# Kernel tuning notes

Hardware: AMD Instinct MI355X
Metric: run time of the kernel (lower is better)

## Reference

```python
import jax, jax.numpy as jnp
import numpy as np

EMB = 512
H1, H2 = 300, 100


def setup_inputs() -> dict:
    key = jax.random.key(0)
    ks = jax.random.split(key, 12)
    B, N, M = 2, 256, 256
    inp = {
        "action_embedding": jax.random.normal(ks[0], (B, EMB, N), jnp.float32),
        "anchor_embedding": jax.random.normal(ks[1], (B, EMB, M), jnp.float32),
        "action_points": jax.random.normal(ks[2], (B, 3, N), jnp.float32),
        "anchor_points": jax.random.normal(ks[3], (B, 3, M), jnp.float32),
        # MLPKernel params: Linear(1024,300), Linear(300,100), Linear(100,1), stored as [in,out]
        "W1": jax.random.normal(ks[4], (2 * EMB, H1), jnp.float32) / np.sqrt(2 * EMB),
        "b1": jax.random.normal(ks[5], (H1,), jnp.float32) * 0.01,
        "W2": jax.random.normal(ks[6], (H1, H2), jnp.float32) / np.sqrt(H1),
        "b2": jax.random.normal(ks[7], (H2,), jnp.float32) * 0.01,
        "W3": jax.random.normal(ks[8], (H2, 1), jnp.float32) / np.sqrt(H2),
        "b3": jax.random.normal(ks[9], (1,), jnp.float32) * 0.01,
    }
    return inp


def _pairwise_radii(Phi_A, Phi_B, W1, b1, W2, b2, W3, b3):
    # MLPKernel: softplus((mlp(cat(a,b)) + mlp(cat(b,a))) / 2) over all (n, m) pairs.
    # Split first linear: cat(x1,x2) @ W1 == x1 @ Wa + x2 @ Wb  (no [B,N,M,1024] materialization).
    F = Phi_A.shape[-1]
    Wa, Wb = W1[:F], W1[F:]
    hA_a = jnp.einsum('bnf,fh->bnh', Phi_A, Wa)
    hA_b = jnp.einsum('bnf,fh->bnh', Phi_A, Wb)
    hB_a = jnp.einsum('bmf,fh->bmh', Phi_B, Wa)
    hB_b = jnp.einsum('bmf,fh->bmh', Phi_B, Wb)

    def mlp_rest(h):  # h: [B,N,M,H1] pre-bias first-layer activations
        h = jax.nn.relu(h + b1)
        h = jax.nn.relu(jnp.einsum('bnmh,hk->bnmk', h, W2) + b2)
        return jnp.einsum('bnmk,ko->bnmo', h, W3) + b3

    v1 = mlp_rest(hA_a[:, :, None, :] + hB_b[:, None, :, :])  # mlp(cat(A_n, B_m))
    v2 = mlp_rest(hB_a[:, None, :, :] + hA_b[:, :, None, :])  # mlp(cat(B_m, A_n))
    return jax.nn.softplus((v1 + v2) * 0.5)[..., 0]  # [B,N,M]


def _multilaterate(P, R, W):
    # Vectorized estimate_p over batch b and query point n.
    # P: [B,M,3] anchor points, R: [B,N,M] estimated radii, W: [B,M] weights.
    M = P.shape[1]
    norm2 = jnp.sum(P * P, axis=-1)                      # [B,M]  (Pt @ P)
    d = norm2[:, None, :] - R ** 2                       # [B,N,M]  PtP - r^2
    a = jnp.einsum('bm,bnm,bmd->bnd', W, d, P) / M       # [B,N,3]
    WPPt = jnp.einsum('bm,bmd,bme->bde', W, P, P) / M    # [B,3,3]  mean(W * P Pt)
    mWd = jnp.einsum('bm,bnm->bn', W, d) / M             # [B,N]    mean(W * (PtP - r^2))
    c = jnp.einsum('bm,bmd->bd', W, P) / M               # [B,3]
    # B @ c with B = -2*mean(W*PPt) - mean(W*d)*I
    Bc = -2.0 * jnp.einsum('bde,be->bd', WPPt, c)[:, None, :] - mWd[..., None] * c[:, None, :]
    cc = jnp.sum(c * c, axis=-1)                         # [B]
    f = a + Bc + 2.0 * cc[:, None, None] * c[:, None, :]  # [B,N,3]
    PPt_mean = jnp.einsum('bmd,bme->bde', P, P) / M       # unweighted mean(PPt)
    H = -2.0 * PPt_mean + 2.0 * jnp.einsum('bd,be->bde', c, c)  # [B,3,3]
    Hinv = jnp.linalg.inv(H)
    q = -jnp.einsum('bde,bne->bnd', Hinv, f)
    return q + c[:, None, :]                              # [B,N,3]


def reference(action_embedding, anchor_embedding, action_points, anchor_points,
              W1, b1, W2, b2, W3, b3):
    P_A = jnp.transpose(action_points, (0, 2, 1))    # [B,N,3]
    P_B = jnp.transpose(anchor_points, (0, 2, 1))    # [B,M,3]
    Phi_A = jnp.transpose(action_embedding, (0, 2, 1))  # [B,N,F]
    Phi_B = jnp.transpose(anchor_embedding, (0, 2, 1))  # [B,M,F]
    B_weights = jnp.ones(Phi_B.shape[:2], dtype=Phi_B.dtype)
    R_est = _pairwise_radii(Phi_A, Phi_B, W1, b1, W2, b2, W3, b3)
    P_A_B_pred = _multilaterate(P_B, R_est, B_weights)  # [B,N,3]
    flow = jnp.transpose(P_A_B_pred - P_A, (0, 2, 1))   # [B,3,N] == full_flow (pred_weight=False)
    return flow
```

## Files before the change

### kernel.cpp

```cpp
#include <hip/hip_runtime.h>
#include <hip/hip_bf16.h>
#include <math.h>

#define EMB 512
#define H1 300
#define H2 100
#define NB 2
#define NN 256
#define MM 256

#define OFF_HAA 0
#define OFF_HAB 153600
#define OFF_HBA 307200
#define OFF_HBB 460800
#define OFF_S   614400
#define OFF_CST 616448
#define OFF_W2C 616512
#define OFF_B2P 634432
#define OFF_W3P 634544
#define OFF_ET  634656
#define OFF_W1T 896800
#define OFF_V   1060640

typedef __attribute__((ext_vector_type(8))) short bf16x8;
typedef __attribute__((ext_vector_type(4))) float f32x4;

static __device__ inline unsigned f2bfbits(float f) {
    union { float f; unsigned u; } v; v.f = f;
    return (v.u + 0x7fffu + ((v.u >> 16) & 1u)) >> 16;
}
static __device__ inline unsigned pack_bf2(float a, float b) {
    union { __hip_bfloat162 h; unsigned u; } cv;
    cv.h = __float22bfloat162_rn(make_float2(a, b));
    return cv.u;
}

__global__ void k_prep(const float* __restrict__ W2, const float* __restrict__ b2,
                       const float* __restrict__ W3, float* __restrict__ ws)
{
    unsigned short* W2c = (unsigned short*)(ws + OFF_W2C);
    int start = blockIdx.x * 256 + threadIdx.x;
    for (int idx = start; idx < 10*112*32; idx += gridDim.x * 256) {
        int c  = idx / 3584;
        int r  = idx - c * 3584;
        int j  = r >> 5;
        int kk = r & 31;
        int k  = c * 32 + kk;
        float v = (j < H2 && k < H1) ? W2[k * H2 + j] : 0.0f;
        W2c[idx] = (unsigned short)f2bfbits(v);
    }
    if (blockIdx.x == 0 && threadIdx.x < 112) {
        int j = threadIdx.x;
        ws[OFF_B2P + j] = (j < H2) ? b2[j] : 0.0f;
        ws[OFF_W3P + j] = (j < H2) ? W3[j] : 0.0f;
    }
}

__global__ void k_prepw1(const float* __restrict__ W1, float* __restrict__ ws)
{
    __shared__ float Tf[32 * 36];
    unsigned short* W1t = (unsigned short*)(ws + OFF_W1T);
    int h0 = blockIdx.x * 32, f0 = blockIdx.y * 32;
    int tid = threadIdx.x;
    int fr = tid >> 3, hc4 = (tid & 7) * 4;
    int hg = h0 + hc4;
    float4 v = make_float4(0.f, 0.f, 0.f, 0.f);
    if (hg < 600) {
        int half = (hg >= 300) ? 1 : 0;
        int hh = hg - half * 300;
        v = *(const float4*)&W1[(size_t)(half * EMB + f0 + fr) * H1 + hh];
    }
    *(float4*)&Tf[fr * 36 + hc4] = v;
    __syncthreads();
    int hr = tid >> 3, f4 = (tid & 7) * 4;
    float v0 = Tf[(f4 + 0) * 36 + hr];
    float v1 = Tf[(f4 + 1) * 36 + hr];
    float v2 = Tf[(f4 + 2) * 36 + hr];
    float v3 = Tf[(f4 + 3) * 36 + hr];
    uint2 pk = make_uint2(pack_bf2(v0, v1), pack_bf2(v2, v3));
    *(uint2*)&W1t[(size_t)(h0 + hr) * EMB + f0 + f4] = pk;
}

__global__ void k_prepe(const float* __restrict__ actE, const float* __restrict__ ancE,
                        float* __restrict__ ws)
{
    __shared__ float Tf[32 * 36];
    unsigned short* Et = (unsigned short*)(ws + OFF_ET);
    int f0 = blockIdx.x * 32, n0 = blockIdx.y * 32;
    int bs = blockIdx.z, b = bs >> 1, src = bs & 1;
    const float* E = (src == 0 ? actE : ancE) + (size_t)b * EMB * NN;
    int tid = threadIdx.x;
    int r = tid >> 3, c4 = (tid & 7) * 4;
    float4 v = *(const float4*)&E[(size_t)(f0 + r) * NN + n0 + c4];
    *(float4*)&Tf[r * 36 + c4] = v;
    __syncthreads();
    int nr = tid >> 3, f4 = (tid & 7) * 4;
    float v0 = Tf[(f4 + 0) * 36 + nr];
    float v1 = Tf[(f4 + 1) * 36 + nr];
    float v2 = Tf[(f4 + 2) * 36 + nr];
    float v3 = Tf[(f4 + 3) * 36 + nr];
    uint2 pk = make_uint2(pack_bf2(v0, v1), pack_bf2(v2, v3));
    *(uint2*)&Et[((size_t)(bs * NN) + n0 + nr) * EMB + f0 + f4] = pk;
}

__global__ void k_const(const float* __restrict__ anchor_pts, float* __restrict__ cst)
{
    int b = blockIdx.x;
    int m = threadIdx.x;
    float px = anchor_pts[b*3*MM + 0*MM + m];
    float py = anchor_pts[b*3*MM + 1*MM + m];
    float pz = anchor_pts[b*3*MM + 2*MM + m];
    float n2 = px*px + py*py + pz*pz;

    float v[13];
    v[0]=px; v[1]=py; v[2]=pz;
    v[3]=px*px; v[4]=px*py; v[5]=px*pz; v[6]=py*py; v[7]=py*pz; v[8]=pz*pz;
    v[9]=n2*px; v[10]=n2*py; v[11]=n2*pz; v[12]=n2;

    #pragma unroll
    for (int off = 32; off >= 1; off >>= 1) {
        #pragma unroll
        for (int i = 0; i < 13; i++) v[i] += __shfl_xor(v[i], off, 64);
    }
    __shared__ float red[4][13];
    int wave = threadIdx.x >> 6, lane = threadIdx.x & 63;
    if (lane == 0) {
        #pragma unroll
        for (int i = 0; i < 13; i++) red[wave][i] = v[i];
    }
    __syncthreads();
    if (threadIdx.x == 0) {
        float s[13];
        #pragma unroll
        for (int i = 0; i < 13; i++)
            s[i] = red[0][i] + red[1][i] + red[2][i] + red[3][i];
        const float invM = 1.0f / MM;
        float c0 = s[0]*invM, c1 = s[1]*invM, c2 = s[2]*invM;
        float Pxx = s[3]*invM, Pxy = s[4]*invM, Pxz = s[5]*invM;
        float Pyy = s[6]*invM, Pyz = s[7]*invM, Pzz = s[8]*invM;

        float H00 = -2.0f*Pxx + 2.0f*c0*c0;
        float H01 = -2.0f*Pxy + 2.0f*c0*c1;
        float H02 = -2.0f*Pxz + 2.0f*c0*c2;
        float H11 = -2.0f*Pyy + 2.0f*c1*c1;
        float H12 = -2.0f*Pyz + 2.0f*c1*c2;
        float H22 = -2.0f*Pzz + 2.0f*c2*c2;
        float H10 = H01, H20 = H02, H21 = H12;

        float det = H00*(H11*H22 - H12*H21)
                  - H01*(H10*H22 - H12*H20)
                  + H02*(H10*H21 - H11*H20);
        float id = 1.0f / det;
        float i00 = (H11*H22 - H12*H21)*id;
        float i01 = (H02*H21 - H01*H22)*id;
        float i02 = (H01*H12 - H02*H11)*id;
        float i10 = (H12*H20 - H10*H22)*id;
        float i11 = (H00*H22 - H02*H20)*id;
        float i12 = (H02*H10 - H00*H12)*id;
        float i20 = (H10*H21 - H11*H20)*id;
        float i21 = (H01*H20 - H00*H21)*id;
        float i22 = (H00*H11 - H01*H10)*id;

        float t0x = -2.0f*(Pxx*c0 + Pxy*c1 + Pxz*c2);
        float t0y = -2.0f*(Pxy*c0 + Pyy*c1 + Pyz*c2);
        float t0z = -2.0f*(Pxz*c0 + Pyz*c1 + Pzz*c2);
        float cc = c0*c0 + c1*c1 + c2*c2;

        float* C = cst + b*32;
        C[0]=c0; C[1]=c1; C[2]=c2;
        C[3]=i00; C[4]=i01; C[5]=i02;
        C[6]=i10; C[7]=i11; C[8]=i12;
        C[9]=i20; C[10]=i21; C[11]=i22;
        C[12]=t0x; C[13]=t0y; C[14]=t0z;
        C[15]=cc;
        C[16]=s[9]*invM; C[17]=s[10]*invM; C[18]=s[11]*invM; C[19]=s[12]*invM;
    }
}

__global__ __launch_bounds__(256) void k_hidden(
    float* __restrict__ ws, const float* __restrict__ b1)
{
    int bs = blockIdx.z, b = bs >> 1, src = bs & 1;
    int n0 = blockIdx.x * 32;
    int h0 = blockIdx.y * 64;
    const unsigned short* Et  = (const unsigned short*)(ws + OFF_ET)
                                + (size_t)(bs * NN) * EMB;
    const unsigned short* W1t = (const unsigned short*)(ws + OFF_W1T);
    float* outA = ws + (src == 0 ? OFF_HAA : OFF_HBA) + (size_t)b * NN * H1;
    float* outB = ws + (src == 0 ? OFF_HAB : OFF_HBB) + (size_t)b * NN * H1;

    __shared__ unsigned short EtL[32 * 40];
    __shared__ unsigned short W1tL[64 * 40];

    int tid = threadIdx.x;
    int lane = tid & 63, w = tid >> 6;
    int colj = lane & 15, quad = lane >> 4;
    int pt = w & 1, jt0 = (w >> 1) * 2;

    int erow = tid >> 3, es4 = (tid & 7) * 4;
    int wrow = tid >> 2, ws8 = (tid & 3) * 8;

    f32x4 acc[2];
    acc[0] = (f32x4){0.f,0.f,0.f,0.f};
    acc[1] = (f32x4){0.f,0.f,0.f,0.f};

    for (int c = 0; c < 16; c++) {
        int k0 = c * 32;
        uint2 ev = *(const uint2*)&Et[(size_t)(n0 + erow) * EMB + k0 + es4];
        uint4 wv = *(const uint4*)&W1t[(size_t)(h0 + wrow) * EMB + k0 + ws8];
        __syncthreads();
        *(uint2*)&EtL[erow * 40 + es4] = ev;
        *(uint4*)&W1tL[wrow * 40 + ws8] = wv;
        __syncthreads();

        bf16x8 af  = *(const bf16x8*)&EtL[(pt * 16 + colj) * 40 + quad * 8];
        bf16x8 bf0 = *(const bf16x8*)&W1tL[(jt0 * 16 + colj) * 40 + quad * 8];
        bf16x8 bf1 = *(const bf16x8*)&W1tL[((jt0 + 1) * 16 + colj) * 40 + quad * 8];
        acc[0] = __builtin_amdgcn_mfma_f32_16x16x32_bf16(af, bf0, acc[0], 0, 0, 0);
        acc[1] = __builtin_amdgcn_mfma_f32_16x16x32_bf16(af, bf1, acc[1], 0, 0, 0);
    }

    #pragma unroll
    for (int j2 = 0; j2 < 2; j2++) {
        int hg = h0 + (jt0 + j2) * 16 + colj;
        if (hg >= 600) continue;
        int hh = (hg < 300) ? hg : hg - 300;
        float* o = (hg < 300) ? outA : outB;
        float bias = (src == 0) ? b1[hh] : 0.0f;
        #pragma unroll
        for (int r = 0; r < 4; r++) {
            int n = n0 + pt * 16 + quad * 4 + r;
            o[(size_t)n * H1 + hh] = acc[j2][r] + bias;
        }
    }
}

__global__ __launch_bounds__(256) void k_pair(
    const float* __restrict__ ws_f, const float* __restrict__ b3p,
    float* __restrict__ V)
{
    int bz = blockIdx.z, b = bz >> 1, p = bz & 1;
    int n0 = blockIdx.y * 16, m0 = blockIdx.x * 16;
    int tid = threadIdx.x;
    int lane = tid & 63, w = tid >> 6;
    int colj = lane & 15, quad = lane >> 4;

    __shared__ float hAfL[16 * 36];
    __shared__ float hBfL[16 * 36];
    __shared__ short W2L[112 * 40];

    const unsigned short* W2c = (const unsigned short*)(ws_f + OFF_W2C);
    float b2v[7], w3v[7];
    #pragma unroll
    for (int jt = 0; jt < 7; jt++) {
        b2v[jt] = ws_f[OFF_B2P + jt * 16 + colj];
        w3v[jt] = ws_f[OFF_W3P + jt * 16 + colj];
    }
    float b3val = b3p[0];

    const float* srcX = ws_f + (p == 0 ? OFF_HAA : OFF_HAB) + (size_t)(b*NN + n0) * H1;
    const float* srcY = ws_f + (p == 0 ? OFF_HBB : OFF_HBA) + (size_t)(b*NN + m0) * H1;

    int sarr = tid >> 7;
    int srow = (tid >> 3) & 15;
    int sseg = tid & 7;
    const float* ssrc = (sarr ? srcY : srcX) + srow * H1;
    float* sdst = (sarr ? hBfL : hAfL) + srow * 36 + sseg * 4;

    f32x4 acc[4][7];
    #pragma unroll
    for (int i = 0; i < 4; i++)
        #pragma unroll
        for (int jt = 0; jt < 7; jt++)
            acc[i][jt] = (f32x4){0.f,0.f,0.f,0.f};

    for (int c = 0; c < 10; c++) {
        float4 sv = *(const float4*)&ssrc[c * 32 + sseg * 4];
        const uint4* wsrc4 = (const uint4*)W2c + c * 448;
        uint4 w0 = wsrc4[tid];
        uint4 w1 = wsrc4[(tid + 256) % 448];

        __syncthreads();
        *(float4*)sdst = sv;
        {
            int j = tid >> 2, q = tid & 3;
            *(uint4*)&W2L[j * 40 + q * 8] = w0;
            if (tid < 192) {
                int u2 = tid + 256;
                *(uint4*)&W2L[(u2 >> 2) * 40 + (u2 & 3) * 8] = w1;
            }
        }
        __syncthreads();

        float4 hb0 = *(const float4*)&hBfL[colj * 36 + quad * 8];
        float4 hb1 = *(const float4*)&hBfL[colj * 36 + quad * 8 + 4];
        bf16x8 bfr[7];
        #pragma unroll
        for (int jt = 0; jt < 7; jt++)
            bfr[jt] = *(const bf16x8*)&W2L[(jt * 16 + colj) * 40 + quad * 8];

        #pragma unroll
        for (int i = 0; i < 4; i++) {
            const float* xa = &hAfL[(w * 4 + i) * 36 + quad * 8];
            float4 ha0 = *(const float4*)&xa[0];
            float4 ha1 = *(const float4*)&xa[4];
            union { unsigned u[4]; bf16x8 v; } af;
            af.u[0] = pack_bf2(fmaxf(ha0.x + hb0.x, 0.f), fmaxf(ha0.y + hb0.y, 0.f));
            af.u[1] = pack_bf2(fmaxf(ha0.z + hb0.z, 0.f), fmaxf(ha0.w + hb0.w, 0.f));
            af.u[2] = pack_bf2(fmaxf(ha1.x + hb1.x, 0.f), fmaxf(ha1.y + hb1.y, 0.f));
            af.u[3] = pack_bf2(fmaxf(ha1.z + hb1.z, 0.f), fmaxf(ha1.w + hb1.w, 0.f));
            #pragma unroll
            for (int jt = 0; jt < 7; jt++)
                acc[i][jt] = __builtin_amdgcn_mfma_f32_16x16x32_bf16(
                    af.v, bfr[jt], acc[i][jt], 0, 0, 0);
        }
    }

    float vsum[4][4];
    #pragma unroll
    for (int i = 0; i < 4; i++)
        #pragma unroll
        for (int r = 0; r < 4; r++) vsum[i][r] = 0.0f;
    #pragma unroll
    for (int i = 0; i < 4; i++)
        #pragma unroll
        for (int jt = 0; jt < 7; jt++)
            #pragma unroll
            for (int r = 0; r < 4; r++)
                vsum[i][r] = fmaf(fmaxf(acc[i][jt][r] + b2v[jt], 0.f),
                                  w3v[jt], vsum[i][r]);

    #pragma unroll
    for (int i = 0; i < 4; i++)
        #pragma unroll
        for (int r = 0; r < 4; r++) {
            float v = vsum[i][r];
            v += __shfl_xor(v, 1, 16);
            v += __shfl_xor(v, 2, 16);
            v += __shfl_xor(v, 4, 16);
            v += __shfl_xor(v, 8, 16);
            vsum[i][r] = v;
        }

    if (colj == 0) {
        #pragma unroll
        for (int i = 0; i < 4; i++) {
            int n = n0 + w * 4 + i;
            float4 o;
            o.x = 0.5f * (vsum[i][0] + b3val);
            o.y = 0.5f * (vsum[i][1] + b3val);
            o.z = 0.5f * (vsum[i][2] + b3val);
            o.w = 0.5f * (vsum[i][3] + b3val);
            *(float4*)&V[(((size_t)p * NB + b) * NN + n) * MM + m0 + quad * 4] = o;
        }
    }
}

__global__ void k_red(const float* __restrict__ V, const float* __restrict__ ancP,
                      float* __restrict__ S)
{
    int b = blockIdx.y;
    int n = blockIdx.x * 16 + (threadIdx.x >> 4);
    int ml = threadIdx.x & 15;
    const float* v0 = V + (((size_t)0 * NB + b) * NN + n) * MM;
    const float* v1 = V + (((size_t)1 * NB + b) * NN + n) * MM;
    float s0 = 0.f, s1 = 0.f, s2 = 0.f, s3 = 0.f;
    #pragma unroll
    for (int k = 0; k < 16; k++) {
        int m = ml + k * 16;
        float x = v0[m] + v1[m];
        float R = fmaxf(x, 0.f) + log1pf(expf(-fabsf(x)));
        float r2 = R * R;
        float px = ancP[b*3*MM + 0*MM + m];
        float py = ancP[b*3*MM + 1*MM + m];
        float pz = ancP[b*3*MM + 2*MM + m];
        s0 = fmaf(r2, px, s0);
        s1 = fmaf(r2, py, s1);
        s2 = fmaf(r2, pz, s2);
        s3 += r2;
    }
    #pragma unroll
    for (int off = 8; off >= 1; off >>= 1) {
        s0 += __shfl_xor(s0, off, 16);
        s1 += __shfl_xor(s1, off, 16);
        s2 += __shfl_xor(s2, off, 16);
        s3 += __shfl_xor(s3, off, 16);
    }
    if (ml == 0) {
        float4 o = make_float4(s0, s1, s2, s3);
        *(float4*)&S[(size_t)(b * NN + n) * 4] = o;
    }
}

__global__ void k_final(const float* __restrict__ S, const float* __restrict__ cst,
                        const float* __restrict__ action_pts, float* __restrict__ out)
{
    int b = blockIdx.x;
    int n = threadIdx.x;
    const float* C = cst + b*32;
    float c0=C[0], c1=C[1], c2=C[2];
    float t0x=C[12], t0y=C[13], t0z=C[14];
    float cc=C[15];
    float SnP0=C[16], SnP1=C[17], SnP2=C[18], Sn=C[19];

    const float* sp = S + (b*NN + n) * 4;
    const float invM = 1.0f / MM;
    float a0 = SnP0 - sp[0]*invM;
    float a1 = SnP1 - sp[1]*invM;
    float a2 = SnP2 - sp[2]*invM;
    float mWd = Sn - sp[3]*invM;

    float f0 = a0 + t0x - mWd*c0 + 2.0f*cc*c0;
    float f1 = a1 + t0y - mWd*c1 + 2.0f*cc*c1;
    float f2 = a2 + t0z - mWd*c2 + 2.0f*cc*c2;

    float q0 = -(C[3]*f0 + C[4]*f1 + C[5]*f2);
    float q1 = -(C[6]*f0 + C[7]*f1 + C[8]*f2);
    float q2 = -(C[9]*f0 + C[10]*f1 + C[11]*f2);

    float p0 = q0 + c0, p1 = q1 + c1, p2 = q2 + c2;

    out[b*3*NN + 0*NN + n] = p0 - action_pts[b*3*NN + 0*NN + n];
    out[b*3*NN + 1*NN + n] = p1 - action_pts[b*3*NN + 1*NN + n];
    out[b*3*NN + 2*NN + n] = p2 - action_pts[b*3*NN + 2*NN + n];
}

extern "C" void kernel_launch(void* const* d_in, const int* in_sizes, int n_in,
                              void* d_out, int out_size, void* d_ws, size_t ws_size,
                              hipStream_t stream)
{
    const float* actE = (const float*)d_in[0];
    const float* ancE = (const float*)d_in[1];
    const float* actP = (const float*)d_in[2];
    const float* ancP = (const float*)d_in[3];
    const float* W1   = (const float*)d_in[4];
    const float* b1   = (const float*)d_in[5];
    const float* W2   = (const float*)d_in[6];
    const float* b2   = (const float*)d_in[7];
    const float* W3   = (const float*)d_in[8];
    const float* b3   = (const float*)d_in[9];
    float* ws  = (float*)d_ws;
    float* out = (float*)d_out;

    k_prep  <<<16, 256, 0, stream>>>(W2, b2, W3, ws);
    k_prepw1<<<dim3(20, 16), 256, 0, stream>>>(W1, ws);
    k_prepe <<<dim3(16, 8, 4), 256, 0, stream>>>(actE, ancE, ws);
    k_const <<<NB, 256, 0, stream>>>(ancP, ws + OFF_CST);
    k_hidden<<<dim3(8, 10, 4), 256, 0, stream>>>(ws, b1);
    k_pair  <<<dim3(16, 16, NB*2), 256, 0, stream>>>(ws, b3, ws + OFF_V);
    k_red   <<<dim3(16, NB), 256, 0, stream>>>(ws + OFF_V, ancP, ws + OFF_S);
    k_final <<<NB, 256, 0, stream>>>(ws + OFF_S, ws + OFF_CST, actP, out);
}
```

Baseline: 132.5 us.

## Merge prep kernels into one launch, fuse reduce+final, shrink hidden tile

Combines the four preprocessing kernels (W1 transpose, embedding transpose, W2 packing, anchor constants) into a single kernel dispatched by block index. It also folds the final multilateration solve into the radius reduction kernel, which removes a launch and the intermediate S buffer. The hidden-layer GEMM tile is halved along n, doubling the block count, with each wave doing one MFMA per step. The main aim is fewer kernel launches and better occupancy, at the cost of less reuse per block in k_hidden.

```diff
diff --git a/kernel.cpp b/kernel.cpp
--- a/kernel.cpp
+++ b/kernel.cpp
@@ -35,145 +35,144 @@
     return cv.u;
 }
 
-__global__ void k_prep(const float* __restrict__ W2, const float* __restrict__ b2,
-                       const float* __restrict__ W3, float* __restrict__ ws)
-{
-    unsigned short* W2c = (unsigned short*)(ws + OFF_W2C);
-    int start = blockIdx.x * 256 + threadIdx.x;
-    for (int idx = start; idx < 10*112*32; idx += gridDim.x * 256) {
-        int c  = idx / 3584;
-        int r  = idx - c * 3584;
-        int j  = r >> 5;
-        int kk = r & 31;
-        int k  = c * 32 + kk;
-        float v = (j < H2 && k < H1) ? W2[k * H2 + j] : 0.0f;
-        W2c[idx] = (unsigned short)f2bfbits(v);
-    }
-    if (blockIdx.x == 0 && threadIdx.x < 112) {
-        int j = threadIdx.x;
-        ws[OFF_B2P + j] = (j < H2) ? b2[j] : 0.0f;
-        ws[OFF_W3P + j] = (j < H2) ? W3[j] : 0.0f;
-    }
-}
-
-__global__ void k_prepw1(const float* __restrict__ W1, float* __restrict__ ws)
+__global__ __launch_bounds__(256) void k_setup(
+    const float* __restrict__ W1, const float* __restrict__ W2,
+    const float* __restrict__ b2, const float* __restrict__ W3,
+    const float* __restrict__ actE, const float* __restrict__ ancE,
+    const float* __restrict__ ancP, float* __restrict__ ws)
 {
     __shared__ float Tf[32 * 36];
-    unsigned short* W1t = (unsigned short*)(ws + OFF_W1T);
-    int h0 = blockIdx.x * 32, f0 = blockIdx.y * 32;
+    __shared__ float red[4][13];
+    int blk = blockIdx.x;
     int tid = threadIdx.x;
-    int fr = tid >> 3, hc4 = (tid & 7) * 4;
-    int hg = h0 + hc4;
-    float4 v = make_float4(0.f, 0.f, 0.f, 0.f);
-    if (hg < 600) {
-        int half = (hg >= 300) ? 1 : 0;
-        int hh = hg - half * 300;
-        v = *(const float4*)&W1[(size_t)(half * EMB + f0 + fr) * H1 + hh];
-    }
-    *(float4*)&Tf[fr * 36 + hc4] = v;
-    __syncthreads();
-    int hr = tid >> 3, f4 = (tid & 7) * 4;
-    float v0 = Tf[(f4 + 0) * 36 + hr];
-    float v1 = Tf[(f4 + 1) * 36 + hr];
-    float v2 = Tf[(f4 + 2) * 36 + hr];
-    float v3 = Tf[(f4 + 3) * 36 + hr];
-    uint2 pk = make_uint2(pack_bf2(v0, v1), pack_bf2(v2, v3));
-    *(uint2*)&W1t[(size_t)(h0 + hr) * EMB + f0 + f4] = pk;
-}
-
-__global__ void k_prepe(const float* __restrict__ actE, const float* __restrict__ ancE,
-                        float* __restrict__ ws)
-{
-    __shared__ float Tf[32 * 36];
-    unsigned short* Et = (unsigned short*)(ws + OFF_ET);
-    int f0 = blockIdx.x * 32, n0 = blockIdx.y * 32;
-    int bs = blockIdx.z, b = bs >> 1, src = bs & 1;
-    const float* E = (src == 0 ? actE : ancE) + (size_t)b * EMB * NN;
-    int tid = threadIdx.x;
-    int r = tid >> 3, c4 = (tid & 7) * 4;
-    float4 v = *(const float4*)&E[(size_t)(f0 + r) * NN + n0 + c4];
-    *(float4*)&Tf[r * 36 + c4] = v;
-    __syncthreads();
-    int nr = tid >> 3, f4 = (tid & 7) * 4;
-    float v0 = Tf[(f4 + 0) * 36 + nr];
-    float v1 = Tf[(f4 + 1) * 36 + nr];
-    float v2 = Tf[(f4 + 2) * 36 + nr];
-    float v3 = Tf[(f4 + 3) * 36 + nr];
-    uint2 pk = make_uint2(pack_bf2(v0, v1), pack_bf2(v2, v3));
-    *(uint2*)&Et[((size_t)(bs * NN) + n0 + nr) * EMB + f0 + f4] = pk;
-}
-
-__global__ void k_const(const float* __restrict__ anchor_pts, float* __restrict__ cst)
-{
-    int b = blockIdx.x;
-    int m = threadIdx.x;
-    float px = anchor_pts[b*3*MM + 0*MM + m];
-    float py = anchor_pts[b*3*MM + 1*MM + m];
-    float pz = anchor_pts[b*3*MM + 2*MM + m];
-    float n2 = px*px + py*py + pz*pz;
-
-    float v[13];
-    v[0]=px; v[1]=py; v[2]=pz;
-    v[3]=px*px; v[4]=px*py; v[5]=px*pz; v[6]=py*py; v[7]=py*pz; v[8]=pz*pz;
-    v[9]=n2*px; v[10]=n2*py; v[11]=n2*pz; v[12]=n2;
-
-    #pragma unroll
-    for (int off = 32; off >= 1; off >>= 1) {
-        #pragma unroll
-        for (int i = 0; i < 13; i++) v[i] += __shfl_xor(v[i], off, 64);
-    }
-    __shared__ float red[4][13];
-    int wave = threadIdx.x >> 6, lane = threadIdx.x & 63;
-    if (lane == 0) {
-        #pragma unroll
-        for (int i = 0; i < 13; i++) red[wave][i] = v[i];
-    }
-    __syncthreads();
-    if (threadIdx.x == 0) {
-        float s[13];
-        #pragma unroll
-        for (int i = 0; i < 13; i++)
-            s[i] = red[0][i] + red[1][i] + red[2][i] + red[3][i];
-        const float invM = 1.0f / MM;
-        float c0 = s[0]*invM, c1 = s[1]*invM, c2 = s[2]*invM;
-        float Pxx = s[3]*invM, Pxy = s[4]*invM, Pxz = s[5]*invM;
-        float Pyy = s[6]*invM, Pyz = s[7]*invM, Pzz = s[8]*invM;
-
-        float H00 = -2.0f*Pxx + 2.0f*c0*c0;
-        float H01 = -2.0f*Pxy + 2.0f*c0*c1;
-        float H02 = -2.0f*Pxz + 2.0f*c0*c2;
-        float H11 = -2.0f*Pyy + 2.0f*c1*c1;
-        float H12 = -2.0f*Pyz + 2.0f*c1*c2;
-        float H22 = -2.0f*Pzz + 2.0f*c2*c2;
-        float H10 = H01, H20 = H02, H21 = H12;
-
-        float det = H00*(H11*H22 - H12*H21)
-                  - H01*(H10*H22 - H12*H20)
-                  + H02*(H10*H21 - H11*H20);
-        float id = 1.0f / det;
-        float i00 = (H11*H22 - H12*H21)*id;
-        float i01 = (H02*H21 - H01*H22)*id;
-        float i02 = (H01*H12 - H02*H11)*id;
-        float i10 = (H12*H20 - H10*H22)*id;
-        float i11 = (H00*H22 - H02*H20)*id;
-        float i12 = (H02*H10 - H00*H12)*id;
-        float i20 = (H10*H21 - H11*H20)*id;
-        float i21 = (H01*H20 - H00*H21)*id;
-        float i22 = (H00*H11 - H01*H10)*id;
-
-        float t0x = -2.0f*(Pxx*c0 + Pxy*c1 + Pxz*c2);
-        float t0y = -2.0f*(Pxy*c0 + Pyy*c1 + Pyz*c2);
-        float t0z = -2.0f*(Pxz*c0 + Pyz*c1 + Pzz*c2);
-        float cc = c0*c0 + c1*c1 + c2*c2;
-
-        float* C = cst + b*32;
-        C[0]=c0; C[1]=c1; C[2]=c2;
-        C[3]=i00; C[4]=i01; C[5]=i02;
-        C[6]=i10; C[7]=i11; C[8]=i12;
-        C[9]=i20; C[10]=i21; C[11]=i22;
-        C[12]=t0x; C[13]=t0y; C[14]=t0z;
-        C[15]=cc;
-        C[16]=s[9]*invM; C[17]=s[10]*invM; C[18]=s[11]*invM; C[19]=s[12]*invM;
+
+    if (blk < 320) {
+        unsigned short* W1t = (unsigned short*)(ws + OFF_W1T);
+        int h0 = (blk % 20) * 32, f0 = (blk / 20) * 32;
+        int fr = tid >> 3, hc4 = (tid & 7) * 4;
+        int hg = h0 + hc4;
+        float4 v = make_float4(0.f, 0.f, 0.f, 0.f);
+        if (hg < 600) {
+            int half = (hg >= 300) ? 1 : 0;
+            int hh = hg - half * 300;
+            v = *(const float4*)&W1[(size_t)(half * EMB + f0 + fr) * H1 + hh];
+        }
+        *(float4*)&Tf[fr * 36 + hc4] = v;
+        __syncthreads();
+        int hr = tid >> 3, f4 = (tid & 7) * 4;
+        float v0 = Tf[(f4 + 0) * 36 + hr];
+        float v1 = Tf[(f4 + 1) * 36 + hr];
+        float v2 = Tf[(f4 + 2) * 36 + hr];
+        float v3 = Tf[(f4 + 3) * 36 + hr];
+        uint2 pk = make_uint2(pack_bf2(v0, v1), pack_bf2(v2, v3));
+        *(uint2*)&W1t[(size_t)(h0 + hr) * EMB + f0 + f4] = pk;
+    } else if (blk < 832) {
+        int i = blk - 320;
+        unsigned short* Et = (unsigned short*)(ws + OFF_ET);
+        int f0 = (i & 15) * 32;
+        int n0 = ((i >> 4) & 7) * 32;
+        int bs = i >> 7, b = bs >> 1, src = bs & 1;
+        const float* E = (src == 0 ? actE : ancE) + (size_t)b * EMB * NN;
+        int r = tid >> 3, c4 = (tid & 7) * 4;
+        float4 v = *(const float4*)&E[(size_t)(f0 + r) * NN + n0 + c4];
+        *(float4*)&Tf[r * 36 + c4] = v;
+        __syncthreads();
+        int nr = tid >> 3, f4 = (tid & 7) * 4;
+        float v0 = Tf[(f4 + 0) * 36 + nr];
+        float v1 = Tf[(f4 + 1) * 36 + nr];
+        float v2 = Tf[(f4 + 2) * 36 + nr];
+        float v3 = Tf[(f4 + 3) * 36 + nr];
+        uint2 pk = make_uint2(pack_bf2(v0, v1), pack_bf2(v2, v3));
+        *(uint2*)&Et[((size_t)(bs * NN) + n0 + nr) * EMB + f0 + f4] = pk;
+    } else if (blk < 848) {
+        int i = blk - 832;
+        unsigned short* W2c = (unsigned short*)(ws + OFF_W2C);
+        int start = i * 256 + tid;
+        for (int idx = start; idx < 10*112*32; idx += 16 * 256) {
+            int c  = idx / 3584;
+            int r  = idx - c * 3584;
+            int j  = r >> 5;
+            int kk = r & 31;
+            int k  = c * 32 + kk;
+            float v = (j < H2 && k < H1) ? W2[k * H2 + j] : 0.0f;
+            W2c[idx] = (unsigned short)f2bfbits(v);
+        }
+        if (i == 0 && tid < 112) {
+            int j = tid;
+            ws[OFF_B2P + j] = (j < H2) ? b2[j] : 0.0f;
+            ws[OFF_W3P + j] = (j < H2) ? W3[j] : 0.0f;
+        }
+    } else {
+        int b = blk - 848;
+        float* cst = ws + OFF_CST;
+        int m = tid;
+        float px = ancP[b*3*MM + 0*MM + m];
+        float py = ancP[b*3*MM + 1*MM + m];
+        float pz = ancP[b*3*MM + 2*MM + m];
+        float n2 = px*px + py*py + pz*pz;
+
+        float v[13];
+        v[0]=px; v[1]=py; v[2]=pz;
+        v[3]=px*px; v[4]=px*py; v[5]=px*pz; v[6]=py*py; v[7]=py*pz; v[8]=pz*pz;
+        v[9]=n2*px; v[10]=n2*py; v[11]=n2*pz; v[12]=n2;
+
+        #pragma unroll
+        for (int off = 32; off >= 1; off >>= 1) {
+            #pragma unroll
+            for (int q = 0; q < 13; q++) v[q] += __shfl_xor(v[q], off, 64);
+        }
+        int wave = tid >> 6, lane = tid & 63;
+        if (lane == 0) {
+            #pragma unroll
+            for (int q = 0; q < 13; q++) red[wave][q] = v[q];
+        }
+        __syncthreads();
+        if (tid == 0) {
+            float s[13];
+            #pragma unroll
+            for (int q = 0; q < 13; q++)
+                s[q] = red[0][q] + red[1][q] + red[2][q] + red[3][q];
+            const float invM = 1.0f / MM;
+            float c0 = s[0]*invM, c1 = s[1]*invM, c2 = s[2]*invM;
+            float Pxx = s[3]*invM, Pxy = s[4]*invM, Pxz = s[5]*invM;
+            float Pyy = s[6]*invM, Pyz = s[7]*invM, Pzz = s[8]*invM;
+
+            float H00 = -2.0f*Pxx + 2.0f*c0*c0;
+            float H01 = -2.0f*Pxy + 2.0f*c0*c1;
+            float H02 = -2.0f*Pxz + 2.0f*c0*c2;
+            float H11 = -2.0f*Pyy + 2.0f*c1*c1;
+            float H12 = -2.0f*Pyz + 2.0f*c1*c2;
+            float H22 = -2.0f*Pzz + 2.0f*c2*c2;
+            float H10 = H01, H20 = H02, H21 = H12;
+
+            float det = H00*(H11*H22 - H12*H21)
+                      - H01*(H10*H22 - H12*H20)
+                      + H02*(H10*H21 - H11*H20);
+            float id = 1.0f / det;
+            float i00 = (H11*H22 - H12*H21)*id;
+            float i01 = (H02*H21 - H01*H22)*id;
+            float i02 = (H01*H12 - H02*H11)*id;
+            float i10 = (H12*H20 - H10*H22)*id;
+            float i11 = (H00*H22 - H02*H20)*id;
+            float i12 = (H02*H10 - H00*H12)*id;
+            float i20 = (H10*H21 - H11*H20)*id;
+            float i21 = (H01*H20 - H00*H21)*id;
+            float i22 = (H00*H11 - H01*H10)*id;
+
+            float t0x = -2.0f*(Pxx*c0 + Pxy*c1 + Pxz*c2);
+            float t0y = -2.0f*(Pxy*c0 + Pyy*c1 + Pyz*c2);
+            float t0z = -2.0f*(Pxz*c0 + Pyz*c1 + Pzz*c2);
+            float cc = c0*c0 + c1*c1 + c2*c2;
+
+            float* C = cst + b*32;
+            C[0]=c0; C[1]=c1; C[2]=c2;
+            C[3]=i00; C[4]=i01; C[5]=i02;
+            C[6]=i10; C[7]=i11; C[8]=i12;
+            C[9]=i20; C[10]=i21; C[11]=i22;
+            C[12]=t0x; C[13]=t0y; C[14]=t0z;
+            C[15]=cc;
+            C[16]=s[9]*invM; C[17]=s[10]*invM; C[18]=s[11]*invM; C[19]=s[12]*invM;
+        }
     }
 }
 
@@ -181,7 +180,7 @@
     float* __restrict__ ws, const float* __restrict__ b1)
 {
     int bs = blockIdx.z, b = bs >> 1, src = bs & 1;
-    int n0 = blockIdx.x * 32;
+    int n0 = blockIdx.x * 16;
     int h0 = blockIdx.y * 64;
     const unsigned short* Et  = (const unsigned short*)(ws + OFF_ET)
                                 + (size_t)(bs * NN) * EMB;
@@ -189,48 +188,40 @@
     float* outA = ws + (src == 0 ? OFF_HAA : OFF_HBA) + (size_t)b * NN * H1;
     float* outB = ws + (src == 0 ? OFF_HAB : OFF_HBB) + (size_t)b * NN * H1;
 
-    __shared__ unsigned short EtL[32 * 40];
+    __shared__ unsigned short EtL[16 * 40];
     __shared__ unsigned short W1tL[64 * 40];
 
     int tid = threadIdx.x;
     int lane = tid & 63, w = tid >> 6;
     int colj = lane & 15, quad = lane >> 4;
-    int pt = w & 1, jt0 = (w >> 1) * 2;
-
-    int erow = tid >> 3, es4 = (tid & 7) * 4;
-    int wrow = tid >> 2, ws8 = (tid & 3) * 8;
-
-    f32x4 acc[2];
-    acc[0] = (f32x4){0.f,0.f,0.f,0.f};
-    acc[1] = (f32x4){0.f,0.f,0.f,0.f};
+
+    int er  = tid >> 4, ek2 = (tid & 15) * 2;
+    int wr  = tid >> 2, wk8 = (tid & 3) * 8;
+
+    f32x4 acc = (f32x4){0.f, 0.f, 0.f, 0.f};
 
     for (int c = 0; c < 16; c++) {
         int k0 = c * 32;
-        uint2 ev = *(const uint2*)&Et[(size_t)(n0 + erow) * EMB + k0 + es4];
-        uint4 wv = *(const uint4*)&W1t[(size_t)(h0 + wrow) * EMB + k0 + ws8];
-        __syncthreads();
-        *(uint2*)&EtL[erow * 40 + es4] = ev;
-        *(uint4*)&W1tL[wrow * 40 + ws8] = wv;
-        __syncthreads();
-
-        bf16x8 af  = *(const bf16x8*)&EtL[(pt * 16 + colj) * 40 + quad * 8];
-        bf16x8 bf0 = *(const bf16x8*)&W1tL[(jt0 * 16 + colj) * 40 + quad * 8];
-        bf16x8 bf1 = *(const bf16x8*)&W1tL[((jt0 + 1) * 16 + colj) * 40 + quad * 8];
-        acc[0] = __builtin_amdgcn_mfma_f32_16x16x32_bf16(af, bf0, acc[0], 0, 0, 0);
-        acc[1] = __builtin_amdgcn_mfma_f32_16x16x32_bf16(af, bf1, acc[1], 0, 0, 0);
-    }
-
-    #pragma unroll
-    for (int j2 = 0; j2 < 2; j2++) {
-        int hg = h0 + (jt0 + j2) * 16 + colj;
-        if (hg >= 600) continue;
+        unsigned ev = *(const unsigned*)&Et[(size_t)(n0 + er) * EMB + k0 + ek2];
+        uint4 wv = *(const uint4*)&W1t[(size_t)(h0 + wr) * EMB + k0 + wk8];
+        __syncthreads();
+        *(unsigned*)&EtL[er * 40 + ek2] = ev;
+        *(uint4*)&W1tL[wr * 40 + wk8] = wv;
+        __syncthreads();
+        bf16x8 af = *(const bf16x8*)&EtL[colj * 40 + quad * 8];
+        bf16x8 bf = *(const bf16x8*)&W1tL[(w * 16 + colj) * 40 + quad * 8];
+        acc = __builtin_amdgcn_mfma_f32_16x16x32_bf16(af, bf, acc, 0, 0, 0);
+    }
+
+    int hg = h0 + w * 16 + colj;
+    if (hg < 600) {
         int hh = (hg < 300) ? hg : hg - 300;
         float* o = (hg < 300) ? outA : outB;
         float bias = (src == 0) ? b1[hh] : 0.0f;
         #pragma unroll
         for (int r = 0; r < 4; r++) {
-            int n = n0 + pt * 16 + quad * 4 + r;
-            o[(size_t)n * H1 + hh] = acc[j2][r] + bias;
+            int n = n0 + quad * 4 + r;
+            o[(size_t)n * H1 + hh] = acc[r] + bias;
         }
     }
 }
@@ -356,8 +347,9 @@
     }
 }
 
-__global__ void k_red(const float* __restrict__ V, const float* __restrict__ ancP,
-                      float* __restrict__ S)
+__global__ void k_finish(const float* __restrict__ V, const float* __restrict__ ancP,
+                         const float* __restrict__ cst, const float* __restrict__ actP,
+                         float* __restrict__ out)
 {
     int b = blockIdx.y;
     int n = blockIdx.x * 16 + (threadIdx.x >> 4);
@@ -387,42 +379,32 @@
         s3 += __shfl_xor(s3, off, 16);
     }
     if (ml == 0) {
-        float4 o = make_float4(s0, s1, s2, s3);
-        *(float4*)&S[(size_t)(b * NN + n) * 4] = o;
-    }
-}
-
-__global__ void k_final(const float* __restrict__ S, const float* __restrict__ cst,
-                        const float* __restrict__ action_pts, float* __restrict__ out)
-{
-    int b = blockIdx.x;
-    int n = threadIdx.x;
-    const float* C = cst + b*32;
-    float c0=C[0], c1=C[1], c2=C[2];
-    float t0x=C[12], t0y=C[13], t0z=C[14];
-    float cc=C[15];
-    float SnP0=C[16], SnP1=C[17], SnP2=C[18], Sn=C[19];
-
-    const float* sp = S + (b*NN + n) * 4;
-    const float invM = 1.0f / MM;
-    float a0 = SnP0 - sp[0]*invM;
-    float a1 = SnP1 - sp[1]*invM;
-    float a2 = SnP2 - sp[2]*invM;
-    float mWd = Sn - sp[3]*invM;
-
-    float f0 = a0 + t0x - mWd*c0 + 2.0f*cc*c0;
-    float f1 = a1 + t0y - mWd*c1 + 2.0f*cc*c1;
-    float f2 = a2 + t0z - mWd*c2 + 2.0f*cc*c2;
-
-    float q0 = -(C[3]*f0 + C[4]*f1 + C[5]*f2);
-    float q1 = -(C[6]*f0 + C[7]*f1 + C[8]*f2);
-    float q2 = -(C[9]*f0 + C[10]*f1 + C[11]*f2);
-
-    float p0 = q0 + c0, p1 = q1 + c1, p2 = q2 + c2;
-
-    out[b*3*NN + 0*NN + n] = p0 - action_pts[b*3*NN + 0*NN + n];
-    out[b*3*NN + 1*NN + n] = p1 - action_pts[b*3*NN + 1*NN + n];
-    out[b*3*NN + 2*NN + n] = p2 - action_pts[b*3*NN + 2*NN + n];
+        const float* C = cst + b*32;
+        float c0=C[0], c1=C[1], c2=C[2];
+        float t0x=C[12], t0y=C[13], t0z=C[14];
+        float cc=C[15];
+        float SnP0=C[16], SnP1=C[17], SnP2=C[18], Sn=C[19];
+
+        const float invM = 1.0f / MM;
+        float a0 = SnP0 - s0*invM;
+        float a1 = SnP1 - s1*invM;
+        float a2 = SnP2 - s2*invM;
+        float mWd = Sn - s3*invM;
+
+        float f0 = a0 + t0x - mWd*c0 + 2.0f*cc*c0;
+        float f1 = a1 + t0y - mWd*c1 + 2.0f*cc*c1;
+        float f2 = a2 + t0z - mWd*c2 + 2.0f*cc*c2;
+
+        float q0 = -(C[3]*f0 + C[4]*f1 + C[5]*f2);
+        float q1 = -(C[6]*f0 + C[7]*f1 + C[8]*f2);
+        float q2 = -(C[9]*f0 + C[10]*f1 + C[11]*f2);
+
+        float p0 = q0 + c0, p1 = q1 + c1, p2 = q2 + c2;
+
+        out[b*3*NN + 0*NN + n] = p0 - actP[b*3*NN + 0*NN + n];
+        out[b*3*NN + 1*NN + n] = p1 - actP[b*3*NN + 1*NN + n];
+        out[b*3*NN + 2*NN + n] = p2 - actP[b*3*NN + 2*NN + n];
+    }
 }
 
 extern "C" void kernel_launch(void* const* d_in, const int* in_sizes, int n_in,
@@ -442,12 +424,8 @@
     float* ws  = (float*)d_ws;
     float* out = (float*)d_out;
 
-    k_prep  <<<16, 256, 0, stream>>>(W2, b2, W3, ws);
-    k_prepw1<<<dim3(20, 16), 256, 0, stream>>>(W1, ws);
-    k_prepe <<<dim3(16, 8, 4), 256, 0, stream>>>(actE, ancE, ws);
-    k_const <<<NB, 256, 0, stream>>>(ancP, ws + OFF_CST);
-    k_hidden<<<dim3(8, 10, 4), 256, 0, stream>>>(ws, b1);
+    k_setup <<<850, 256, 0, stream>>>(W1, W2, b2, W3, actE, ancE, ancP, ws);
+    k_hidden<<<dim3(16, 10, 4), 256, 0, stream>>>(ws, b1);
     k_pair  <<<dim3(16, 16, NB*2), 256, 0, stream>>>(ws, b3, ws + OFF_V);
-    k_red   <<<dim3(16, NB), 256, 0, stream>>>(ws + OFF_V, ancP, ws + OFF_S);
-    k_final <<<NB, 256, 0, stream>>>(ws + OFF_S, ws + OFF_CST, actP, out);
-}
+    k_finish<<<dim3(16, NB), 256, 0, stream>>>(ws + OFF_V, ancP, ws + OFF_CST, actP, out);
+}
```

Result: faster. 126.4 us (-4.6%).
